# Performance work log

Hardware: AMD Instinct MI355X
Metric: run time of the kernel (lower is better)

Reference implementation:

```python
import jax, jax.numpy as jnp
import numpy as np

B, K, T, H = 64, 49, 512, 512  # batch, regions, timesteps, hidden_size
A = 49                          # attention bottleneck dim (hard-coded in module)


def setup_inputs() -> dict:
    key = jax.random.key(0)
    ks = jax.random.split(key, 7)
    s = 1.0 / np.sqrt(H)
    return {
        "V":   jax.random.normal(ks[0], (B, K, H), jnp.float32),
        "h_t": jax.random.normal(ks[1], (B, T, H), jnp.float32),
        "s_t": jax.random.normal(ks[2], (B, T, H), jnp.float32),
        "Wv":  jax.random.normal(ks[3], (A, H), jnp.float32) * s,
        "Wg":  jax.random.normal(ks[4], (A, H), jnp.float32) * s,
        "Ws":  jax.random.normal(ks[5], (A, H), jnp.float32) * s,
        "Wh":  jax.random.normal(ks[6], (1, A), jnp.float32) * (1.0 / np.sqrt(A)),
    }


def reference(V, h_t, s_t, Wv, Wg, Ws, Wh):
    # Dropout is identity (eval mode). torch.nn.Linear: y = x @ W.T
    wh = Wh[0]                                     # [A]
    cv = jnp.einsum('bkh,ah->bka', V, Wv)          # [B,K,A]
    gh = jnp.einsum('bth,ah->bta', h_t, Wg)        # [B,T,A]
    content_v = cv[:, None, :, :] + gh[:, :, None, :]      # [B,T,K,A]
    z_t = jnp.einsum('btka,a->btk', jnp.tanh(content_v), wh)  # [B,T,K]
    alpha_t = jax.nn.softmax(z_t, axis=-1)         # softmax over K regions
    c_t = jnp.einsum('btk,bkh->bth', alpha_t, V)   # [B,T,H]

    content_s = jnp.einsum('bth,ah->bta', s_t, Ws) + gh       # [B,T,A]
    z_ext = jnp.einsum('bta,a->bt', jnp.tanh(content_s), wh)  # [B,T]
    extended = jnp.concatenate([z_t, z_ext[:, :, None]], axis=2)  # [B,T,K+1]
    alpha_hat = jax.nn.softmax(extended, axis=-1)
    beta_t = alpha_hat[:, :, -1:]                  # [B,T,1] sentinel gate

    c_hat_t = beta_t * s_t + (1.0 - beta_t) * c_t  # [B,T,H]
    return c_hat_t, alpha_t, beta_t
```

## Files before the change

### kernel.cpp

```cpp
#include <hip/hip_runtime.h>
#include <hip/hip_bf16.h>
#include <cstdint>
#include <cstddef>

#define NB 64
#define NK 49
#define NT 512
#define NH 512
#define NA 49

typedef __attribute__((ext_vector_type(8))) short bf16x8;
typedef __attribute__((ext_vector_type(4))) float f32x4;

__device__ __forceinline__ float fast_exp(float x) {
    return __builtin_amdgcn_exp2f(x * 1.4426950408889634f);
}
__device__ __forceinline__ float fast_tanh(float x) {
    float e = __builtin_amdgcn_exp2f(x * 2.8853900817779268f);
    return 1.0f - 2.0f * __builtin_amdgcn_rcpf(e + 1.0f);
}
__device__ __forceinline__ short bf16rn(float x) {
    unsigned b = __builtin_bit_cast(unsigned, x);
    unsigned r = b + 0x7FFFu + ((b >> 16) & 1u);
    return (short)(r >> 16);
}
__device__ __forceinline__ void split_hi_lo(float x, short& hi, short& lo) {
    unsigned b = __builtin_bit_cast(unsigned, x);
    unsigned hb = b & 0xFFFF0000u;
    hi = (short)(hb >> 16);
    lo = bf16rn(x - __builtin_bit_cast(float, hb));
}

__global__ void kprep(const float* __restrict__ Wg, const float* __restrict__ Ws,
                      const float* __restrict__ Wv, short* __restrict__ WB) {
    const int job = blockIdx.x >> 3, slice = blockIdx.x & 7;
    const float* W = (job == 0) ? Wg : (job == 1 ? Ws : Wv);
    short* dst = WB + (size_t)job * 65536;
    const int end = (slice + 1) * 8192;
    for (int idx = slice * 8192 + threadIdx.x; idx < end; idx += 256) {
        int e    = idx & 7;
        int lane = (idx >> 3) & 63;
        int ks   = (idx >> 9) & 15;
        int nt   = (idx >> 13) & 3;
        int sel  = idx >> 15;
        int a = nt * 16 + (lane & 15);
        int h = ks * 32 + (lane >> 4) * 8 + e;
        float x = (a < NA) ? W[a * NH + h] : 0.0f;
        short hi, lo; split_hi_lo(x, hi, lo);
        dst[idx] = sel ? lo : hi;
    }
}

__global__ __launch_bounds__(256, 8) void kvprep(const float* __restrict__ V,
                                                 short* __restrict__ VB) {
    __shared__ float vl[NK * 64];
    const int b  = blockIdx.x >> 3;
    const int sl = blockIdx.x & 7;
    const int h0 = sl * 64;
    const float* Vb = V + (size_t)b * (NK * NH);

    for (int idx = threadIdx.x; idx < NK * 64; idx += 256) {
        int k = idx >> 6, c = idx & 63;
        vl[idx] = Vb[(size_t)k * NH + h0 + c];
    }
    __syncthreads();

    short* dst = VB + (size_t)b * 32768;
    for (int idx = threadIdx.x; idx < 4096; idx += 256) {
        int e    = idx & 7;
        int lane = (idx >> 3) & 63;
        int ks   = (idx >> 9) & 1;
        int ntl  = idx >> 10;
        int k = ks * 32 + (lane >> 4) * 8 + e;
        int c = ntl * 16 + (lane & 15);
        float x = (k < NK) ? vl[k * 64 + c] : 0.0f;
        dst[((size_t)(sl * 4 + ntl) * 2 + ks) * 512 + lane * 8 + e] = bf16rn(x);
    }
}

__global__ __launch_bounds__(256, 4) void kcv(
        const float* __restrict__ V, const short* __restrict__ WB,
        float* __restrict__ cv) {
    const int tid  = threadIdx.x;
    const int lane = tid & 63;
    const int w    = tid >> 6;
    const int m0   = blockIdx.x * 64 + w * 16;
    const int r    = lane & 15;
    const int g    = lane >> 4;

    const float* arow = V + (size_t)(m0 + r) * NH + g * 8;
    const bf16x8* wbv = (const bf16x8*)(WB + 2 * 65536);

    f32x4 acc0 = {0.f, 0.f, 0.f, 0.f};
    f32x4 acc1 = acc0, acc2 = acc0, acc3 = acc0;

    #pragma unroll 2
    for (int ks = 0; ks < 16; ++ks) {
        float4 x0 = *(const float4*)(arow + ks * 32);
        float4 x1 = *(const float4*)(arow + ks * 32 + 4);
        bf16x8 bh0 = wbv[(0 * 16 + ks) * 64 + lane];
        bf16x8 bh1 = wbv[(1 * 16 + ks) * 64 + lane];
        bf16x8 bh2 = wbv[(2 * 16 + ks) * 64 + lane];
        bf16x8 bh3 = wbv[(3 * 16 + ks) * 64 + lane];
        bf16x8 bl0 = wbv[(4 * 16 + ks) * 64 + lane];
        bf16x8 bl1 = wbv[(5 * 16 + ks) * 64 + lane];
        bf16x8 bl2 = wbv[(6 * 16 + ks) * 64 + lane];
        bf16x8 bl3 = wbv[(7 * 16 + ks) * 64 + lane];

        bf16x8 ahi, alo;
        {
            const float xs[8] = {x0.x, x0.y, x0.z, x0.w, x1.x, x1.y, x1.z, x1.w};
            #pragma unroll
            for (int e = 0; e < 8; ++e) { short hi, lo; split_hi_lo(xs[e], hi, lo); ahi[e] = hi; alo[e] = lo; }
        }
        acc0 = __builtin_amdgcn_mfma_f32_16x16x32_bf16(ahi, bh0, acc0, 0, 0, 0);
        acc0 = __builtin_amdgcn_mfma_f32_16x16x32_bf16(alo, bh0, acc0, 0, 0, 0);
        acc0 = __builtin_amdgcn_mfma_f32_16x16x32_bf16(ahi, bl0, acc0, 0, 0, 0);
        acc1 = __builtin_amdgcn_mfma_f32_16x16x32_bf16(ahi, bh1, acc1, 0, 0, 0);
        acc1 = __builtin_amdgcn_mfma_f32_16x16x32_bf16(alo, bh1, acc1, 0, 0, 0);
        acc1 = __builtin_amdgcn_mfma_f32_16x16x32_bf16(ahi, bl1, acc1, 0, 0, 0);
        acc2 = __builtin_amdgcn_mfma_f32_16x16x32_bf16(ahi, bh2, acc2, 0, 0, 0);
        acc2 = __builtin_amdgcn_mfma_f32_16x16x32_bf16(alo, bh2, acc2, 0, 0, 0);
        acc2 = __builtin_amdgcn_mfma_f32_16x16x32_bf16(ahi, bl2, acc2, 0, 0, 0);
        acc3 = __builtin_amdgcn_mfma_f32_16x16x32_bf16(ahi, bh3, acc3, 0, 0, 0);
        acc3 = __builtin_amdgcn_mfma_f32_16x16x32_bf16(alo, bh3, acc3, 0, 0, 0);
        acc3 = __builtin_amdgcn_mfma_f32_16x16x32_bf16(ahi, bl3, acc3, 0, 0, 0);
    }

    #pragma unroll
    for (int reg = 0; reg < 4; ++reg) {
        int row = m0 + g * 4 + reg;
        float* orow = cv + (size_t)row * NA;
        orow[ 0 + r] = acc0[reg];
        orow[16 + r] = acc1[reg];
        orow[32 + r] = acc2[reg];
        if (r == 0) orow[48] = acc3[reg];
    }
}

__global__ __launch_bounds__(256, 4) void kfused(
        const float* __restrict__ h_t, const float* __restrict__ s_t,
        const float* __restrict__ Wh,
        const short* __restrict__ WB, const short* __restrict__ VB,
        const float* __restrict__ cv_ws,
        float* __restrict__ out_chat, float* __restrict__ out_alpha,
        float* __restrict__ out_beta) {
    __shared__ float cvl[NK * 52];
    __shared__ float ghl[32 * 52];
    __shared__ float ssl[32 * 52];
    __shared__ float zl[32 * 50];
    __shared__ short afrag[2048];
    __shared__ float whl[52];
    __shared__ float betal[32];

    const int tid  = threadIdx.x;
    const int lane = tid & 63;
    const int w    = tid >> 6;
    const int b    = blockIdx.x >> 4;
    const int t0   = (blockIdx.x & 15) * 32;
    const int r    = lane & 15;
    const int g    = lane >> 4;

    {
        const float* cvb = cv_ws + (size_t)b * (NK * NA);
        for (int idx = tid; idx < NK * NA; idx += 256) {
            int k = idx / NA, a = idx - k * NA;
            cvl[k * 52 + a] = cvb[idx];
        }
        if (tid < NA) whl[tid] = Wh[tid];
    }

    {
        const int job = w >> 1, mtile = w & 1;
        const float* in = job ? s_t : h_t;
        const bf16x8* wb = (const bf16x8*)(WB + (size_t)job * 65536);
        const float* arow = in + (size_t)(b * NT + t0 + mtile * 16 + r) * NH + g * 8;
        f32x4 acc0 = {0.f, 0.f, 0.f, 0.f};
        f32x4 acc1 = acc0, acc2 = acc0, acc3 = acc0;
        #pragma unroll 2
        for (int ks = 0; ks < 16; ++ks) {
            float4 x0 = *(const float4*)(arow + ks * 32);
            float4 x1 = *(const float4*)(arow + ks * 32 + 4);
            bf16x8 bh0 = wb[(( 0 + 0) * 16 + ks) * 64 + lane];
            bf16x8 bh1 = wb[(( 0 + 1) * 16 + ks) * 64 + lane];
            bf16x8 bh2 = wb[(( 0 + 2) * 16 + ks) * 64 + lane];
            bf16x8 bh3 = wb[(( 0 + 3) * 16 + ks) * 64 + lane];
            bf16x8 bl0 = wb[(( 4 + 0) * 16 + ks) * 64 + lane];
            bf16x8 bl1 = wb[(( 4 + 1) * 16 + ks) * 64 + lane];
            bf16x8 bl2 = wb[(( 4 + 2) * 16 + ks) * 64 + lane];
            bf16x8 bl3 = wb[(( 4 + 3) * 16 + ks) * 64 + lane];
            bf16x8 ahi, alo;
            {
                const float xs[8] = {x0.x, x0.y, x0.z, x0.w, x1.x, x1.y, x1.z, x1.w};
                #pragma unroll
                for (int e = 0; e < 8; ++e) { short hi, lo; split_hi_lo(xs[e], hi, lo); ahi[e] = hi; alo[e] = lo; }
            }
            acc0 = __builtin_amdgcn_mfma_f32_16x16x32_bf16(ahi, bh0, acc0, 0, 0, 0);
            acc0 = __builtin_amdgcn_mfma_f32_16x16x32_bf16(alo, bh0, acc0, 0, 0, 0);
            acc0 = __builtin_amdgcn_mfma_f32_16x16x32_bf16(ahi, bl0, acc0, 0, 0, 0);
            acc1 = __builtin_amdgcn_mfma_f32_16x16x32_bf16(ahi, bh1, acc1, 0, 0, 0);
            acc1 = __builtin_amdgcn_mfma_f32_16x16x32_bf16(alo, bh1, acc1, 0, 0, 0);
            acc1 = __builtin_amdgcn_mfma_f32_16x16x32_bf16(ahi, bl1, acc1, 0, 0, 0);
            acc2 = __builtin_amdgcn_mfma_f32_16x16x32_bf16(ahi, bh2, acc2, 0, 0, 0);
            acc2 = __builtin_amdgcn_mfma_f32_16x16x32_bf16(alo, bh2, acc2, 0, 0, 0);
            acc2 = __builtin_amdgcn_mfma_f32_16x16x32_bf16(ahi, bl2, acc2, 0, 0, 0);
            acc3 = __builtin_amdgcn_mfma_f32_16x16x32_bf16(ahi, bh3, acc3, 0, 0, 0);
            acc3 = __builtin_amdgcn_mfma_f32_16x16x32_bf16(alo, bh3, acc3, 0, 0, 0);
            acc3 = __builtin_amdgcn_mfma_f32_16x16x32_bf16(ahi, bl3, acc3, 0, 0, 0);
        }
        float* dst = (w >> 1) ? ssl : ghl;
        #pragma unroll
        for (int reg = 0; reg < 4; ++reg) {
            int m = mtile * 16 + g * 4 + reg;
            dst[m * 52 +  0 + r] = acc0[reg];
            dst[m * 52 + 16 + r] = acc1[reg];
            dst[m * 52 + 32 + r] = acc2[reg];
            if (r < 4) dst[m * 52 + 48 + r] = acc3[reg];
        }
    }
    __syncthreads();

    {
        const float w48 = whl[48];
        for (int p = tid; p < 32 * 50; p += 256) {
            int t = p / 50, kk = p - t * 50;
            const float* rowp = (kk < NK) ? (cvl + kk * 52) : (ssl + t * 52);
            const float* gp = ghl + t * 52;
            float z = 0.0f;
            #pragma unroll
            for (int q = 0; q < 12; ++q) {
                float4 rr = *(const float4*)(rowp + q * 4);
                float4 gg = *(const float4*)(gp + q * 4);
                z = fmaf(whl[q * 4 + 0], fast_tanh(rr.x + gg.x), z);
                z = fmaf(whl[q * 4 + 1], fast_tanh(rr.y + gg.y), z);
                z = fmaf(whl[q * 4 + 2], fast_tanh(rr.z + gg.z), z);
                z = fmaf(whl[q * 4 + 3], fast_tanh(rr.w + gg.w), z);
            }
            z = fmaf(w48, fast_tanh(rowp[48] + gp[48]), z);
            zl[p] = z;
        }
    }
    __syncthreads();

    if (tid < 32) {
        const float* zr = zl + tid * 50;
        float m49 = -1e30f;
        #pragma unroll
        for (int k = 0; k < NK; ++k) m49 = fmaxf(m49, zr[k]);
        float S = 0.0f;
        #pragma unroll
        for (int k = 0; k < NK; ++k) S += fast_exp(zr[k] - m49);
        float rS = __builtin_amdgcn_rcpf(S);

        float ze   = zr[49];
        float m50  = fmaxf(m49, ze);
        float eext = fast_exp(ze - m50);
        float beta = eext * __builtin_amdgcn_rcpf(S * fast_exp(m49 - m50) + eext);
        betal[tid] = beta;
        out_beta[(size_t)b * NT + t0 + tid] = beta;

        float* al = ghl + tid * 50;
        const int mt = tid >> 4, rr2 = tid & 15;
        for (int k = 0; k < 64; ++k) {
            float a = (k < NK) ? fast_exp(zr[k] - m49) * rS : 0.0f;
            if (k < NK) al[k] = a;
            int ks = k >> 5, gg = (k & 31) >> 3, e = k & 7;
            int ln = gg * 16 + rr2;
            afrag[((ks * 2 + mt) * 64 + ln) * 8 + e] = bf16rn(a);
        }
    }
    __syncthreads();

    {
        float* oa = out_alpha + ((size_t)b * NT + t0) * NK;
        for (int idx = tid; idx < 32 * NK; idx += 256) {
            int t = idx / NK, k = idx - t * NK;
            oa[idx] = ghl[t * 50 + k];
        }
    }

    {
        const bf16x8* af = (const bf16x8*)afrag;
        const bf16x8* vb = (const bf16x8*)(VB + (size_t)b * 32768);
        const size_t rowb = (size_t)b * NT + t0;

        bf16x8 a00 = af[(0 * 2 + 0) * 64 + lane];
        bf16x8 a01 = af[(0 * 2 + 1) * 64 + lane];
        bf16x8 a10 = af[(1 * 2 + 0) * 64 + lane];
        bf16x8 a11 = af[(1 * 2 + 1) * 64 + lane];

        #pragma unroll 2
        for (int ntl = 0; ntl < 8; ++ntl) {
            const int nt = w * 8 + ntl;
            bf16x8 b0 = vb[(nt * 2 + 0) * 64 + lane];
            bf16x8 b1 = vb[(nt * 2 + 1) * 64 + lane];
            f32x4 acc0 = {0.f, 0.f, 0.f, 0.f};
            f32x4 acc1 = acc0;
            acc0 = __builtin_amdgcn_mfma_f32_16x16x32_bf16(a00, b0, acc0, 0, 0, 0);
            acc0 = __builtin_amdgcn_mfma_f32_16x16x32_bf16(a10, b1, acc0, 0, 0, 0);
            acc1 = __builtin_amdgcn_mfma_f32_16x16x32_bf16(a01, b0, acc1, 0, 0, 0);
            acc1 = __builtin_amdgcn_mfma_f32_16x16x32_bf16(a11, b1, acc1, 0, 0, 0);

            const int h0 = nt * 16 + r;
            #pragma unroll
            for (int reg = 0; reg < 4; ++reg) {
                {
                    int tloc = g * 4 + reg;
                    float bt = betal[tloc];
                    size_t off = (rowb + tloc) * NH + h0;
                    float s = s_t[off];
                    out_chat[off] = fmaf(bt, s - acc0[reg], acc0[reg]);
                }
                {
                    int tloc = 16 + g * 4 + reg;
                    float bt = betal[tloc];
                    size_t off = (rowb + tloc) * NH + h0;
                    float s = s_t[off];
                    out_chat[off] = fmaf(bt, s - acc1[reg], acc1[reg]);
                }
            }
        }
    }
}

extern "C" void kernel_launch(void* const* d_in, const int* in_sizes, int n_in,
                              void* d_out, int out_size, void* d_ws, size_t ws_size,
                              hipStream_t stream) {
    const float* V   = (const float*)d_in[0];
    const float* h_t = (const float*)d_in[1];
    const float* s_t = (const float*)d_in[2];
    const float* Wv  = (const float*)d_in[3];
    const float* Wg  = (const float*)d_in[4];
    const float* Ws  = (const float*)d_in[5];
    const float* Wh  = (const float*)d_in[6];

    float* out = (float*)d_out;
    float* out_chat  = out;
    float* out_alpha = out + (size_t)NB * NT * NH;
    float* out_beta  = out_alpha + (size_t)NB * NT * NK;

    short* WB = (short*)d_ws;
    short* VB = WB + (size_t)3 * 65536;
    float* cv = (float*)(VB + (size_t)64 * 32768);

    kprep<<<24, 256, 0, stream>>>(Wg, Ws, Wv, WB);
    kvprep<<<NB * 8, 256, 0, stream>>>(V, VB);
    kcv<<<49, 256, 0, stream>>>(V, WB, cv);
    kfused<<<NB * 16, 256, 0, stream>>>(h_t, s_t, Wh, WB, VB, cv,
                                        out_chat, out_alpha, out_beta);
}
```

Baseline: 103.9 us.

## Read cv directly from global, parallelize softmax across all threads, raise occupancy

Drops the shared-memory staging of the per-batch cv tile. The z computation now reads cv rows straight from a padded (stride-52) global workspace, which frees LDS and allows launch bounds of 6 blocks per SM. The softmax/alpha stage now uses all 256 threads, with 8 lanes per timestep and shuffle reductions, instead of 32 serial threads. The trade-off is that z now reads cv from global/L2 repeatedly, and the tighter register budget may cause spills.

```diff
diff --git a/kernel.cpp b/kernel.cpp
--- a/kernel.cpp
+++ b/kernel.cpp
@@ -29,6 +29,21 @@
     unsigned hb = b & 0xFFFF0000u;
     hi = (short)(hb >> 16);
     lo = bf16rn(x - __builtin_bit_cast(float, hb));
+}
+
+template <typename PtrT>
+__device__ __forceinline__ float zdot(PtrT rowp, const float* gp, const float* whl) {
+    float z = 0.0f;
+    #pragma unroll
+    for (int q = 0; q < 12; ++q) {
+        float4 rr = *(const float4*)(rowp + q * 4);
+        float4 gg = *(const float4*)(gp + q * 4);
+        z = fmaf(whl[q * 4 + 0], fast_tanh(rr.x + gg.x), z);
+        z = fmaf(whl[q * 4 + 1], fast_tanh(rr.y + gg.y), z);
+        z = fmaf(whl[q * 4 + 2], fast_tanh(rr.z + gg.z), z);
+        z = fmaf(whl[q * 4 + 3], fast_tanh(rr.w + gg.w), z);
+    }
+    return fmaf(whl[48], fast_tanh(rowp[48] + gp[48]), z);
 }
 
 __global__ void kprep(const float* __restrict__ Wg, const float* __restrict__ Ws,
@@ -130,7 +145,7 @@
     #pragma unroll
     for (int reg = 0; reg < 4; ++reg) {
         int row = m0 + g * 4 + reg;
-        float* orow = cv + (size_t)row * NA;
+        float* orow = cv + (size_t)row * 52;
         orow[ 0 + r] = acc0[reg];
         orow[16 + r] = acc1[reg];
         orow[32 + r] = acc2[reg];
@@ -138,14 +153,13 @@
     }
 }
 
-__global__ __launch_bounds__(256, 4) void kfused(
+__global__ __launch_bounds__(256, 6) void kfused(
         const float* __restrict__ h_t, const float* __restrict__ s_t,
         const float* __restrict__ Wh,
         const short* __restrict__ WB, const short* __restrict__ VB,
         const float* __restrict__ cv_ws,
         float* __restrict__ out_chat, float* __restrict__ out_alpha,
         float* __restrict__ out_beta) {
-    __shared__ float cvl[NK * 52];
     __shared__ float ghl[32 * 52];
     __shared__ float ssl[32 * 52];
     __shared__ float zl[32 * 50];
@@ -161,14 +175,7 @@
     const int r    = lane & 15;
     const int g    = lane >> 4;
 
-    {
-        const float* cvb = cv_ws + (size_t)b * (NK * NA);
-        for (int idx = tid; idx < NK * NA; idx += 256) {
-            int k = idx / NA, a = idx - k * NA;
-            cvl[k * 52 + a] = cvb[idx];
-        }
-        if (tid < NA) whl[tid] = Wh[tid];
-    }
+    if (tid < NA) whl[tid] = Wh[tid];
 
     {
         const int job = w >> 1, mtile = w & 1;
@@ -221,52 +228,52 @@
     __syncthreads();
 
     {
-        const float w48 = whl[48];
+        const float* cvb = cv_ws + (size_t)b * (NK * 52);
         for (int p = tid; p < 32 * 50; p += 256) {
             int t = p / 50, kk = p - t * 50;
-            const float* rowp = (kk < NK) ? (cvl + kk * 52) : (ssl + t * 52);
             const float* gp = ghl + t * 52;
-            float z = 0.0f;
-            #pragma unroll
-            for (int q = 0; q < 12; ++q) {
-                float4 rr = *(const float4*)(rowp + q * 4);
-                float4 gg = *(const float4*)(gp + q * 4);
-                z = fmaf(whl[q * 4 + 0], fast_tanh(rr.x + gg.x), z);
-                z = fmaf(whl[q * 4 + 1], fast_tanh(rr.y + gg.y), z);
-                z = fmaf(whl[q * 4 + 2], fast_tanh(rr.z + gg.z), z);
-                z = fmaf(whl[q * 4 + 3], fast_tanh(rr.w + gg.w), z);
-            }
-            z = fmaf(w48, fast_tanh(rowp[48] + gp[48]), z);
+            float z;
+            if (kk < NK) z = zdot(cvb + (size_t)kk * 52, gp, whl);
+            else         z = zdot(ssl + t * 52, gp, whl);
             zl[p] = z;
         }
     }
     __syncthreads();
 
-    if (tid < 32) {
-        const float* zr = zl + tid * 50;
-        float m49 = -1e30f;
-        #pragma unroll
-        for (int k = 0; k < NK; ++k) m49 = fmaxf(m49, zr[k]);
+    {
+        const int trow = w * 8 + (lane >> 3);
+        const int sub  = lane & 7;
+        const float* zr = zl + trow * 50;
+
+        float m = -1e30f;
+        for (int k = sub; k < NK; k += 8) m = fmaxf(m, zr[k]);
+        m = fmaxf(m, __shfl_xor(m, 1));
+        m = fmaxf(m, __shfl_xor(m, 2));
+        m = fmaxf(m, __shfl_xor(m, 4));
+
         float S = 0.0f;
-        #pragma unroll
-        for (int k = 0; k < NK; ++k) S += fast_exp(zr[k] - m49);
+        for (int k = sub; k < NK; k += 8) S += fast_exp(zr[k] - m);
+        S += __shfl_xor(S, 1);
+        S += __shfl_xor(S, 2);
+        S += __shfl_xor(S, 4);
         float rS = __builtin_amdgcn_rcpf(S);
 
         float ze   = zr[49];
-        float m50  = fmaxf(m49, ze);
+        float m50  = fmaxf(m, ze);
         float eext = fast_exp(ze - m50);
-        float beta = eext * __builtin_amdgcn_rcpf(S * fast_exp(m49 - m50) + eext);
-        betal[tid] = beta;
-        out_beta[(size_t)b * NT + t0 + tid] = beta;
-
-        float* al = ghl + tid * 50;
-        const int mt = tid >> 4, rr2 = tid & 15;
-        for (int k = 0; k < 64; ++k) {
-            float a = (k < NK) ? fast_exp(zr[k] - m49) * rS : 0.0f;
+        float beta = eext * __builtin_amdgcn_rcpf(S * fast_exp(m - m50) + eext);
+        if (sub == 0) {
+            betal[trow] = beta;
+            out_beta[(size_t)b * NT + t0 + trow] = beta;
+        }
+
+        float* al = ghl + trow * 50;
+        const int mt = trow >> 4, rr2 = trow & 15;
+        for (int k = sub; k < 64; k += 8) {
+            float a = (k < NK) ? fast_exp(zr[k] - m) * rS : 0.0f;
             if (k < NK) al[k] = a;
-            int ks = k >> 5, gg = (k & 31) >> 3, e = k & 7;
-            int ln = gg * 16 + rr2;
-            afrag[((ks * 2 + mt) * 64 + ln) * 8 + e] = bf16rn(a);
+            int ks = k >> 5, gg = (k & 31) >> 3;
+            afrag[(((ks * 2 + mt) * 64) + gg * 16 + rr2) * 8 + sub] = bf16rn(a);
         }
     }
     __syncthreads();
```

Result: slower. 139.8 us (+34.5%).
